# Kernel optimization log

Hardware: AMD Instinct MI355X
Metric: run time of the kernel (lower is better)

The kernel has to match this reference:

```python
import jax, jax.numpy as jnp
import numpy as np

N0 = 260000  # all sampled nodes (hop-2 sources)
N1 = 60000   # hop-1 targets / hop-2 sources
N2 = 10000   # final batch targets
E1 = 1500000
E2 = 250000
DIN, DH, DOUT = 128, 256, 128


def sage_conv(x_src, x_tgt, src, dst, n_tgt, Wl, b, Wr):
    # mean aggregation of source features over incoming edges per target,
    # then lin_l(agg) + lin_r(x_tgt)  (PyG SAGEConv default, lin_r has no bias)
    msg = x_src[src]                                             # [E, d]
    agg = jax.ops.segment_sum(msg, dst, num_segments=n_tgt)      # [n_tgt, d]
    cnt = jax.ops.segment_sum(jnp.ones((src.shape[0], 1), x_src.dtype), dst,
                              num_segments=n_tgt)                # [n_tgt, 1]
    agg = agg / jnp.maximum(cnt, 1.0)
    return agg @ Wl + b + x_tgt @ Wr


def setup_inputs() -> dict:
    key = jax.random.key(0)
    ks = jax.random.split(key, 10)
    s = 1.0 / np.sqrt(DIN)
    s2 = 1.0 / np.sqrt(DH)
    return {
        "x": jax.random.normal(ks[0], (N0, DIN), dtype=jnp.float32),
        "W1l": jax.random.normal(ks[1], (DIN, DH), dtype=jnp.float32) * s,
        "b1": jnp.zeros((DH,), dtype=jnp.float32),
        "W1r": jax.random.normal(ks[2], (DIN, DH), dtype=jnp.float32) * s,
        "W2l": jax.random.normal(ks[3], (DH, DOUT), dtype=jnp.float32) * s2,
        "b2": jnp.zeros((DOUT,), dtype=jnp.float32),
        "W2r": jax.random.normal(ks[4], (DH, DOUT), dtype=jnp.float32) * s2,
        "src1": jax.random.randint(ks[5], (E1,), 0, N0, dtype=jnp.int32),
        "dst1": jax.random.randint(ks[6], (E1,), 0, N1, dtype=jnp.int32),
        "src2": jax.random.randint(ks[7], (E2,), 0, N1, dtype=jnp.int32),
        "dst2": jax.random.randint(ks[8], (E2,), 0, N2, dtype=jnp.int32),
    }


def reference(x, W1l, b1, W1r, W2l, b2, W2r, src1, dst1, src2, dst2):
    h = sage_conv(x, x[:N1], src1, dst1, N1, W1l, b1, W1r)  # [N1, DH]
    h = jax.nn.relu(h)
    out = sage_conv(h, h[:N2], src2, dst2, N2, W2l, b2, W2r)  # [N2, DOUT]
    return out
```

## Files before the change

### kernel.cpp

```cpp
#include <hip/hip_runtime.h>
#include <hip/hip_bf16.h>

#define N0 260000
#define N1 60000
#define N2 10000
#define E1 1500000
#define E2 250000
#define DIN 128
#define DH 256
#define DOUT 128
#define CAP 80

typedef __attribute__((ext_vector_type(8))) short bf16x8;
typedef __attribute__((ext_vector_type(4))) float f32x4;

#define MFMA16(a, b, c) __builtin_amdgcn_mfma_f32_16x16x32_bf16(a, b, c, 0, 0, 0)

__device__ inline float blo(unsigned u) { return __uint_as_float(u << 16); }
__device__ inline float bhi(unsigned u) { return __uint_as_float(u & 0xFFFF0000u); }
__device__ inline unsigned short f2b(float f) {
    unsigned u = __float_as_uint(f);
    return (unsigned short)((u + 0x7FFFu + ((u >> 16) & 1u)) >> 16);
}

#define CONVX_BLOCKS 16250
#define CONVW_BLOCKS 512
__global__ __launch_bounds__(256) void prep2(const float* __restrict__ x, unsigned short* __restrict__ xb,
                                             const float* __restrict__ W1l, const float* __restrict__ W1r,
                                             const float* __restrict__ W2l, const float* __restrict__ W2r,
                                             unsigned short* __restrict__ W1lt, unsigned short* __restrict__ W1rt,
                                             unsigned short* __restrict__ W2lt, unsigned short* __restrict__ W2rt,
                                             int use_xb) {
    int b = blockIdx.x;
    int t = threadIdx.x;
    if (b < CONVX_BLOCKS) {
        if (!use_xb) return;
        size_t i = (size_t)b * 256 + t;
        const float4* xf = reinterpret_cast<const float4*>(x) + i * 2;
        float4 v0 = xf[0], v1 = xf[1];
        bf16x8 o;
        o[0] = (short)f2b(v0.x); o[1] = (short)f2b(v0.y); o[2] = (short)f2b(v0.z); o[3] = (short)f2b(v0.w);
        o[4] = (short)f2b(v1.x); o[5] = (short)f2b(v1.y); o[6] = (short)f2b(v1.z); o[7] = (short)f2b(v1.w);
        *reinterpret_cast<bf16x8*>(xb + i * 8) = o;
    } else {
        int tid = (b - CONVX_BLOCKS) * 256 + t;
        int seg = tid >> 15, idx = tid & 32767;
        if (seg == 0)      { int n = idx >> 7, k = idx & 127; W1lt[idx] = f2b(W1l[k * DH + n]); }
        else if (seg == 1) { int n = idx >> 7, k = idx & 127; W1rt[idx] = f2b(W1r[k * DH + n]); }
        else if (seg == 2) { int n = idx >> 8, k = idx & 255; W2lt[idx] = f2b(W2l[k * DOUT + n]); }
        else               { int n = idx >> 8, k = idx & 255; W2rt[idx] = f2b(W2r[k * DOUT + n]); }
    }
}

#define BB_C1 256
#define BB_C2 64
#define P1ROWS (N1 / 8)
#define P2ROWS (N2 / 8)
__global__ __launch_bounds__(256) void build_bucket(const int* __restrict__ src1, const int* __restrict__ dst1,
                                                    int* __restrict__ cnt1, int* __restrict__ csr1,
                                                    const int* __restrict__ src2, const int* __restrict__ dst2,
                                                    int* __restrict__ cnt2, int* __restrict__ csr2) {
    int b = blockIdx.x;
    int part = b & 7, q = b >> 3;
    int t = threadIdx.x;
    if (q < BB_C1) {
        int lo = part * P1ROWS, hi = lo + P1ROWS;
        const int4* d4 = reinterpret_cast<const int4*>(dst1);
        for (int i = q * 256 + t; i < E1 / 4; i += BB_C1 * 256) {
            int4 d = d4[i];
            int e0 = i * 4;
            if (d.x >= lo && d.x < hi) { int p = atomicAdd(&cnt1[d.x], 1); if (p < CAP) csr1[d.x * CAP + p] = src1[e0 + 0]; }
            if (d.y >= lo && d.y < hi) { int p = atomicAdd(&cnt1[d.y], 1); if (p < CAP) csr1[d.y * CAP + p] = src1[e0 + 1]; }
            if (d.z >= lo && d.z < hi) { int p = atomicAdd(&cnt1[d.z], 1); if (p < CAP) csr1[d.z * CAP + p] = src1[e0 + 2]; }
            if (d.w >= lo && d.w < hi) { int p = atomicAdd(&cnt1[d.w], 1); if (p < CAP) csr1[d.w * CAP + p] = src1[e0 + 3]; }
        }
    } else {
        q -= BB_C1;
        int lo = part * P2ROWS, hi = lo + P2ROWS;
        const int4* d4 = reinterpret_cast<const int4*>(dst2);
        for (int i = q * 256 + t; i < E2 / 4; i += BB_C2 * 256) {
            int4 d = d4[i];
            int e0 = i * 4;
            if (d.x >= lo && d.x < hi) { int p = atomicAdd(&cnt2[d.x], 1); if (p < CAP) csr2[d.x * CAP + p] = src2[e0 + 0]; }
            if (d.y >= lo && d.y < hi) { int p = atomicAdd(&cnt2[d.y], 1); if (p < CAP) csr2[d.y * CAP + p] = src2[e0 + 1]; }
            if (d.z >= lo && d.z < hi) { int p = atomicAdd(&cnt2[d.z], 1); if (p < CAP) csr2[d.z * CAP + p] = src2[e0 + 2]; }
            if (d.w >= lo && d.w < hi) { int p = atomicAdd(&cnt2[d.w], 1); if (p < CAP) csr2[d.w * CAP + p] = src2[e0 + 3]; }
        }
    }
}

template <int XB>
__global__ __launch_bounds__(256) void agg_gemm1_k(const float* __restrict__ xf,
                                                   const unsigned short* __restrict__ xb,
                                                   const int* __restrict__ cnt,
                                                   const int* __restrict__ csr,
                                                   const unsigned short* __restrict__ Wlt,
                                                   const unsigned short* __restrict__ Wrt,
                                                   const float* __restrict__ b1,
                                                   unsigned short* __restrict__ hb) {
    __shared__ __align__(16) unsigned short lds[4352];
    const int XT0 = 2176;
    int t = threadIdx.x;
    int row0 = blockIdx.x * 16;
    int r = t >> 4, li = t & 15;
    int rawc = cnt[row0 + r];
    int deg = rawc > CAP ? CAP : rawc;
    int beg = (row0 + r) * CAP, end = beg + deg;
    float acc[8];
#pragma unroll
    for (int j = 0; j < 8; ++j) acc[j] = 0.0f;
    if (XB) {
        const uint4* base = reinterpret_cast<const uint4*>(xb);
        int e = beg;
        for (; e + 4 <= end; e += 4) {
            int s0 = csr[e + 0];
            int s1 = csr[e + 1];
            int s2 = csr[e + 2];
            int s3 = csr[e + 3];
            uint4 v0 = base[(size_t)s0 * 16 + li];
            uint4 v1 = base[(size_t)s1 * 16 + li];
            uint4 v2 = base[(size_t)s2 * 16 + li];
            uint4 v3 = base[(size_t)s3 * 16 + li];
            acc[0] += blo(v0.x) + blo(v1.x) + blo(v2.x) + blo(v3.x);
            acc[1] += bhi(v0.x) + bhi(v1.x) + bhi(v2.x) + bhi(v3.x);
            acc[2] += blo(v0.y) + blo(v1.y) + blo(v2.y) + blo(v3.y);
            acc[3] += bhi(v0.y) + bhi(v1.y) + bhi(v2.y) + bhi(v3.y);
            acc[4] += blo(v0.z) + blo(v1.z) + blo(v2.z) + blo(v3.z);
            acc[5] += bhi(v0.z) + bhi(v1.z) + bhi(v2.z) + bhi(v3.z);
            acc[6] += blo(v0.w) + blo(v1.w) + blo(v2.w) + blo(v3.w);
            acc[7] += bhi(v0.w) + bhi(v1.w) + bhi(v2.w) + bhi(v3.w);
        }
        for (; e < end; ++e) {
            int s = csr[e];
            uint4 v = base[(size_t)s * 16 + li];
            acc[0] += blo(v.x); acc[1] += bhi(v.x);
            acc[2] += blo(v.y); acc[3] += bhi(v.y);
            acc[4] += blo(v.z); acc[5] += bhi(v.z);
            acc[6] += blo(v.w); acc[7] += bhi(v.w);
        }
    } else {
        const float4* base = reinterpret_cast<const float4*>(xf);
        for (int e = beg; e < end; ++e) {
            int s = csr[e];
            float4 v0 = base[(size_t)s * 32 + li * 2];
            float4 v1 = base[(size_t)s * 32 + li * 2 + 1];
            acc[0] += v0.x; acc[1] += v0.y; acc[2] += v0.z; acc[3] += v0.w;
            acc[4] += v1.x; acc[5] += v1.y; acc[6] += v1.z; acc[7] += v1.w;
        }
    }
    float inv = 1.0f / fmaxf((float)rawc, 1.0f);
    bf16x8 av;
#pragma unroll
    for (int j = 0; j < 8; ++j) av[j] = (short)f2b(acc[j] * inv);
    *reinterpret_cast<bf16x8*>(&lds[r * 136 + li * 8]) = av;
    if (XB) {
        *reinterpret_cast<uint4*>(&lds[XT0 + r * 136 + li * 8]) =
            reinterpret_cast<const uint4*>(xb)[(size_t)(row0 + r) * 16 + li];
    } else {
        const float4* base = reinterpret_cast<const float4*>(xf);
        float4 v0 = base[(size_t)(row0 + r) * 32 + li * 2];
        float4 v1 = base[(size_t)(row0 + r) * 32 + li * 2 + 1];
        bf16x8 xv;
        xv[0] = (short)f2b(v0.x); xv[1] = (short)f2b(v0.y); xv[2] = (short)f2b(v0.z); xv[3] = (short)f2b(v0.w);
        xv[4] = (short)f2b(v1.x); xv[5] = (short)f2b(v1.y); xv[6] = (short)f2b(v1.z); xv[7] = (short)f2b(v1.w);
        *reinterpret_cast<bf16x8*>(&lds[XT0 + r * 136 + li * 8]) = xv;
    }
    __syncthreads();

    int l = t & 63, w = t >> 6;
    f32x4 c[4];
#pragma unroll
    for (int nt = 0; nt < 4; ++nt) c[nt] = (f32x4){0.f, 0.f, 0.f, 0.f};
    int arow = (l & 15) * 136;
    int colbase = w * 64 + (l & 15);
    int kbase = (l >> 4) * 8;
#pragma unroll
    for (int kk = 0; kk < 4; ++kk) {
        int goff = arow + (kk * 4 + (l >> 4)) * 8;
        bf16x8 af = *reinterpret_cast<const bf16x8*>(&lds[goff]);
        bf16x8 tf = *reinterpret_cast<const bf16x8*>(&lds[XT0 + goff]);
        int k = kk * 32 + kbase;
#pragma unroll
        for (int nt = 0; nt < 4; ++nt) {
            int n = colbase + nt * 16;
            bf16x8 wl = *reinterpret_cast<const bf16x8*>(&Wlt[n * DIN + k]);
            bf16x8 wr = *reinterpret_cast<const bf16x8*>(&Wrt[n * DIN + k]);
            c[nt] = MFMA16(af, wl, c[nt]);
            c[nt] = MFMA16(tf, wr, c[nt]);
        }
    }
    __syncthreads();
#pragma unroll
    for (int nt = 0; nt < 4; ++nt) {
        int col = colbase + nt * 16;
        float bias = b1[col];
#pragma unroll
        for (int j = 0; j < 4; ++j) {
            int rr = (l >> 4) * 4 + j;
            lds[rr * 264 + col] = f2b(fmaxf(c[nt][j] + bias, 0.0f));
        }
    }
    __syncthreads();
#pragma unroll
    for (int i = 0; i < 2; ++i) {
        int gi = t + i * 256;
        int rr = gi >> 5, g = gi & 31;
        *reinterpret_cast<uint4*>(&hb[(size_t)(row0 + rr) * 256 + g * 8]) =
            *reinterpret_cast<const uint4*>(&lds[rr * 264 + g * 8]);
    }
}

__global__ __launch_bounds__(512) void agg_gemm2_k(const unsigned short* __restrict__ hb,
                                                   const int* __restrict__ cnt,
                                                   const int* __restrict__ csr,
                                                   const unsigned short* __restrict__ Wlt,
                                                   const unsigned short* __restrict__ Wrt,
                                                   const float* __restrict__ b2,
                                                   float* __restrict__ out) {
    __shared__ __align__(16) unsigned short lds[8448];
    const int HT0 = 4224;
    int t = threadIdx.x;
    int row0 = blockIdx.x * 16;
    int r = t >> 5, li = t & 31;
    int rawc = cnt[row0 + r];
    int deg = rawc > CAP ? CAP : rawc;
    int beg = (row0 + r) * CAP, end = beg + deg;
    float acc[8];
#pragma unroll
    for (int j = 0; j < 8; ++j) acc[j] = 0.0f;
    const uint4* base = reinterpret_cast<const uint4*>(hb);
    int e = beg;
    for (; e + 4 <= end; e += 4) {
        int s0 = csr[e + 0];
        int s1 = csr[e + 1];
        int s2 = csr[e + 2];
        int s3 = csr[e + 3];
        uint4 v0 = base[(size_t)s0 * 32 + li];
        uint4 v1 = base[(size_t)s1 * 32 + li];
        uint4 v2 = base[(size_t)s2 * 32 + li];
        uint4 v3 = base[(size_t)s3 * 32 + li];
        acc[0] += blo(v0.x) + blo(v1.x) + blo(v2.x) + blo(v3.x);
        acc[1] += bhi(v0.x) + bhi(v1.x) + bhi(v2.x) + bhi(v3.x);
        acc[2] += blo(v0.y) + blo(v1.y) + blo(v2.y) + blo(v3.y);
        acc[3] += bhi(v0.y) + bhi(v1.y) + bhi(v2.y) + bhi(v3.y);
        acc[4] += blo(v0.z) + blo(v1.z) + blo(v2.z) + blo(v3.z);
        acc[5] += bhi(v0.z) + bhi(v1.z) + bhi(v2.z) + bhi(v3.z);
        acc[6] += blo(v0.w) + blo(v1.w) + blo(v2.w) + blo(v3.w);
        acc[7] += bhi(v0.w) + bhi(v1.w) + bhi(v2.w) + bhi(v3.w);
    }
    for (; e < end; ++e) {
        int s = csr[e];
        uint4 v = base[(size_t)s * 32 + li];
        acc[0] += blo(v.x); acc[1] += bhi(v.x);
        acc[2] += blo(v.y); acc[3] += bhi(v.y);
        acc[4] += blo(v.z); acc[5] += bhi(v.z);
        acc[6] += blo(v.w); acc[7] += bhi(v.w);
    }
    float inv = 1.0f / fmaxf((float)rawc, 1.0f);
    bf16x8 av;
#pragma unroll
    for (int j = 0; j < 8; ++j) av[j] = (short)f2b(acc[j] * inv);
    *reinterpret_cast<bf16x8*>(&lds[r * 264 + li * 8]) = av;
    *reinterpret_cast<uint4*>(&lds[HT0 + r * 264 + li * 8]) =
        reinterpret_cast<const uint4*>(&hb[(size_t)(row0 + r) * 256])[li];
    __syncthreads();

    int l = t & 63, w = t >> 6;
    f32x4 c = (f32x4){0.f, 0.f, 0.f, 0.f};
    int arow = (l & 15) * 264;
    int col = w * 16 + (l & 15);
    int kbase = (l >> 4) * 8;
#pragma unroll
    for (int kk = 0; kk < 8; ++kk) {
        int goff = arow + (kk * 4 + (l >> 4)) * 8;
        bf16x8 af = *reinterpret_cast<const bf16x8*>(&lds[goff]);
        bf16x8 hf = *reinterpret_cast<const bf16x8*>(&lds[HT0 + goff]);
        int k = kk * 32 + kbase;
        bf16x8 wl = *reinterpret_cast<const bf16x8*>(&Wlt[col * DH + k]);
        bf16x8 wr = *reinterpret_cast<const bf16x8*>(&Wrt[col * DH + k]);
        c = MFMA16(af, wl, c);
        c = MFMA16(hf, wr, c);
    }
    __syncthreads();
    float* O = reinterpret_cast<float*>(lds);
    float bias = b2[col];
#pragma unroll
    for (int j = 0; j < 4; ++j) {
        int rr = (l >> 4) * 4 + j;
        O[rr * 132 + col] = c[j] + bias;
    }
    __syncthreads();
    {
        int rr = t >> 5, c4 = t & 31;
        reinterpret_cast<float4*>(&out[(size_t)(row0 + rr) * 128])[c4] =
            reinterpret_cast<const float4*>(O)[rr * 33 + c4];
    }
}

extern "C" void kernel_launch(void* const* d_in, const int* in_sizes, int n_in,
                              void* d_out, int out_size, void* d_ws, size_t ws_size,
                              hipStream_t stream) {
    const float* x   = (const float*)d_in[0];
    const float* W1l = (const float*)d_in[1];
    const float* b1  = (const float*)d_in[2];
    const float* W1r = (const float*)d_in[3];
    const float* W2l = (const float*)d_in[4];
    const float* b2  = (const float*)d_in[5];
    const float* W2r = (const float*)d_in[6];
    const int* src1  = (const int*)d_in[7];
    const int* dst1  = (const int*)d_in[8];
    const int* src2  = (const int*)d_in[9];
    const int* dst2  = (const int*)d_in[10];
    float* out = (float*)d_out;

    char* ws = (char*)d_ws;
    size_t off = 0;
    auto alloc = [&](size_t bytes) { void* p = ws + off; off += (bytes + 255) & ~(size_t)255; return p; };
    int* cnt1    = (int*)alloc((size_t)N1 * 4);
    int* cnt2    = (int*)alloc((size_t)N2 * 4);
    int* csr1    = (int*)alloc((size_t)N1 * CAP * 4);
    int* csr2    = (int*)alloc((size_t)N2 * CAP * 4);
    unsigned short* W1lt = (unsigned short*)alloc((size_t)DIN * DH * 2);
    unsigned short* W1rt = (unsigned short*)alloc((size_t)DIN * DH * 2);
    unsigned short* W2lt = (unsigned short*)alloc((size_t)DH * DOUT * 2);
    unsigned short* W2rt = (unsigned short*)alloc((size_t)DH * DOUT * 2);
    unsigned short* hb   = (unsigned short*)alloc((size_t)N1 * DH * 2);
    unsigned short* xb   = (unsigned short*)alloc((size_t)N0 * DIN * 2);
    int use_xb = (off <= ws_size) ? 1 : 0;

    hipMemsetAsync(cnt1, 0, (size_t)((char*)cnt2 - (char*)cnt1) + (size_t)N2 * 4, stream);

    prep2<<<CONVX_BLOCKS + CONVW_BLOCKS, 256, 0, stream>>>(
        x, xb, W1l, W1r, W2l, W2r, W1lt, W1rt, W2lt, W2rt, use_xb);

    build_bucket<<<8 * (BB_C1 + BB_C2), 256, 0, stream>>>(src1, dst1, cnt1, csr1,
                                                          src2, dst2, cnt2, csr2);

    if (use_xb)
        agg_gemm1_k<1><<<N1 / 16, 256, 0, stream>>>(x, xb, cnt1, csr1, W1lt, W1rt, b1, hb);
    else
        agg_gemm1_k<0><<<N1 / 16, 256, 0, stream>>>(x, nullptr, cnt1, csr1, W1lt, W1rt, b1, hb);

    agg_gemm2_k<<<N2 / 16, 512, 0, stream>>>(hb, cnt2, csr2, W2lt, W2rt, b2, out);
}
```

Baseline: 256.5 us.

## Fuse bucket build into prep kernel and widen gather unroll to eight edges

The CSR bucket-building work now runs as the leading blocks of the prep kernel, so the atomic scatter overlaps with the bf16 conversion of x and the weights, and one launch and its inter-kernel gap go away. Both aggregation kernels now read neighbour indices as int4 vectors and issue eight row gathers per iteration instead of four, with a four-edge tail step, to put more memory loads in flight. The vector index loads rely on each row's CSR slot being 16-byte aligned, which holds because CAP is 80. The wider unroll raises register use, which could lower occupancy.

Result: faster. 248.7 us (-3.1%).

```diff
diff --git a/kernel.cpp b/kernel.cpp
--- a/kernel.cpp
+++ b/kernel.cpp
@@ -23,19 +23,54 @@
     return (unsigned short)((u + 0x7FFFu + ((u >> 16) & 1u)) >> 16);
 }
 
+#define BB_C1 256
+#define BB_C2 64
+#define BB_BLOCKS (8 * (BB_C1 + BB_C2))
+#define P1ROWS (N1 / 8)
+#define P2ROWS (N2 / 8)
 #define CONVX_BLOCKS 16250
 #define CONVW_BLOCKS 512
-__global__ __launch_bounds__(256) void prep2(const float* __restrict__ x, unsigned short* __restrict__ xb,
+__global__ __launch_bounds__(256) void prep3(const float* __restrict__ x, unsigned short* __restrict__ xb,
                                              const float* __restrict__ W1l, const float* __restrict__ W1r,
                                              const float* __restrict__ W2l, const float* __restrict__ W2r,
                                              unsigned short* __restrict__ W1lt, unsigned short* __restrict__ W1rt,
                                              unsigned short* __restrict__ W2lt, unsigned short* __restrict__ W2rt,
+                                             const int* __restrict__ src1, const int* __restrict__ dst1,
+                                             int* __restrict__ cnt1, int* __restrict__ csr1,
+                                             const int* __restrict__ src2, const int* __restrict__ dst2,
+                                             int* __restrict__ cnt2, int* __restrict__ csr2,
                                              int use_xb) {
     int b = blockIdx.x;
     int t = threadIdx.x;
-    if (b < CONVX_BLOCKS) {
+    if (b < BB_BLOCKS) {
+        int part = b & 7, q = b >> 3;
+        if (q < BB_C1) {
+            int lo = part * P1ROWS, hi = lo + P1ROWS;
+            const int4* d4 = reinterpret_cast<const int4*>(dst1);
+            for (int i = q * 256 + t; i < E1 / 4; i += BB_C1 * 256) {
+                int4 d = d4[i];
+                int e0 = i * 4;
+                if (d.x >= lo && d.x < hi) { int p = atomicAdd(&cnt1[d.x], 1); if (p < CAP) csr1[d.x * CAP + p] = src1[e0 + 0]; }
+                if (d.y >= lo && d.y < hi) { int p = atomicAdd(&cnt1[d.y], 1); if (p < CAP) csr1[d.y * CAP + p] = src1[e0 + 1]; }
+                if (d.z >= lo && d.z < hi) { int p = atomicAdd(&cnt1[d.z], 1); if (p < CAP) csr1[d.z * CAP + p] = src1[e0 + 2]; }
+                if (d.w >= lo && d.w < hi) { int p = atomicAdd(&cnt1[d.w], 1); if (p < CAP) csr1[d.w * CAP + p] = src1[e0 + 3]; }
+            }
+        } else {
+            q -= BB_C1;
+            int lo = part * P2ROWS, hi = lo + P2ROWS;
+            const int4* d4 = reinterpret_cast<const int4*>(dst2);
+            for (int i = q * 256 + t; i < E2 / 4; i += BB_C2 * 256) {
+                int4 d = d4[i];
+                int e0 = i * 4;
+                if (d.x >= lo && d.x < hi) { int p = atomicAdd(&cnt2[d.x], 1); if (p < CAP) csr2[d.x * CAP + p] = src2[e0 + 0]; }
+                if (d.y >= lo && d.y < hi) { int p = atomicAdd(&cnt2[d.y], 1); if (p < CAP) csr2[d.y * CAP + p] = src2[e0 + 1]; }
+                if (d.z >= lo && d.z < hi) { int p = atomicAdd(&cnt2[d.z], 1); if (p < CAP) csr2[d.z * CAP + p] = src2[e0 + 2]; }
+                if (d.w >= lo && d.w < hi) { int p = atomicAdd(&cnt2[d.w], 1); if (p < CAP) csr2[d.w * CAP + p] = src2[e0 + 3]; }
+            }
+        }
+    } else if (b < BB_BLOCKS + CONVX_BLOCKS) {
         if (!use_xb) return;
-        size_t i = (size_t)b * 256 + t;
+        size_t i = (size_t)(b - BB_BLOCKS) * 256 + t;
         const float4* xf = reinterpret_cast<const float4*>(x) + i * 2;
         float4 v0 = xf[0], v1 = xf[1];
         bf16x8 o;
@@ -43,49 +78,12 @@
         o[4] = (short)f2b(v1.x); o[5] = (short)f2b(v1.y); o[6] = (short)f2b(v1.z); o[7] = (short)f2b(v1.w);
         *reinterpret_cast<bf16x8*>(xb + i * 8) = o;
     } else {
-        int tid = (b - CONVX_BLOCKS) * 256 + t;
+        int tid = (b - BB_BLOCKS - CONVX_BLOCKS) * 256 + t;
         int seg = tid >> 15, idx = tid & 32767;
         if (seg == 0)      { int n = idx >> 7, k = idx & 127; W1lt[idx] = f2b(W1l[k * DH + n]); }
         else if (seg == 1) { int n = idx >> 7, k = idx & 127; W1rt[idx] = f2b(W1r[k * DH + n]); }
         else if (seg == 2) { int n = idx >> 8, k = idx & 255; W2lt[idx] = f2b(W2l[k * DOUT + n]); }
         else               { int n = idx >> 8, k = idx & 255; W2rt[idx] = f2b(W2r[k * DOUT + n]); }
-    }
-}
-
-#define BB_C1 256
-#define BB_C2 64
-#define P1ROWS (N1 / 8)
-#define P2ROWS (N2 / 8)
-__global__ __launch_bounds__(256) void build_bucket(const int* __restrict__ src1, const int* __restrict__ dst1,
-                                                    int* __restrict__ cnt1, int* __restrict__ csr1,
-                                                    const int* __restrict__ src2, const int* __restrict__ dst2,
-                                                    int* __restrict__ cnt2, int* __restrict__ csr2) {
-    int b = blockIdx.x;
-    int part = b & 7, q = b >> 3;
-    int t = threadIdx.x;
-    if (q < BB_C1) {
-        int lo = part * P1ROWS, hi = lo + P1ROWS;
-        const int4* d4 = reinterpret_cast<const int4*>(dst1);
-        for (int i = q * 256 + t; i < E1 / 4; i += BB_C1 * 256) {
-            int4 d = d4[i];
-            int e0 = i * 4;
-            if (d.x >= lo && d.x < hi) { int p = atomicAdd(&cnt1[d.x], 1); if (p < CAP) csr1[d.x * CAP + p] = src1[e0 + 0]; }
-            if (d.y >= lo && d.y < hi) { int p = atomicAdd(&cnt1[d.y], 1); if (p < CAP) csr1[d.y * CAP + p] = src1[e0 + 1]; }
-            if (d.z >= lo && d.z < hi) { int p = atomicAdd(&cnt1[d.z], 1); if (p < CAP) csr1[d.z * CAP + p] = src1[e0 + 2]; }
-            if (d.w >= lo && d.w < hi) { int p = atomicAdd(&cnt1[d.w], 1); if (p < CAP) csr1[d.w * CAP + p] = src1[e0 + 3]; }
-        }
-    } else {
-        q -= BB_C1;
-        int lo = part * P2ROWS, hi = lo + P2ROWS;
-        const int4* d4 = reinterpret_cast<const int4*>(dst2);
-        for (int i = q * 256 + t; i < E2 / 4; i += BB_C2 * 256) {
-            int4 d = d4[i];
-            int e0 = i * 4;
-            if (d.x >= lo && d.x < hi) { int p = atomicAdd(&cnt2[d.x], 1); if (p < CAP) csr2[d.x * CAP + p] = src2[e0 + 0]; }
-            if (d.y >= lo && d.y < hi) { int p = atomicAdd(&cnt2[d.y], 1); if (p < CAP) csr2[d.y * CAP + p] = src2[e0 + 1]; }
-            if (d.z >= lo && d.z < hi) { int p = atomicAdd(&cnt2[d.z], 1); if (p < CAP) csr2[d.z * CAP + p] = src2[e0 + 2]; }
-            if (d.w >= lo && d.w < hi) { int p = atomicAdd(&cnt2[d.w], 1); if (p < CAP) csr2[d.w * CAP + p] = src2[e0 + 3]; }
-        }
     }
 }
 
@@ -112,15 +110,32 @@
     if (XB) {
         const uint4* base = reinterpret_cast<const uint4*>(xb);
         int e = beg;
-        for (; e + 4 <= end; e += 4) {
-            int s0 = csr[e + 0];
-            int s1 = csr[e + 1];
-            int s2 = csr[e + 2];
-            int s3 = csr[e + 3];
-            uint4 v0 = base[(size_t)s0 * 16 + li];
-            uint4 v1 = base[(size_t)s1 * 16 + li];
-            uint4 v2 = base[(size_t)s2 * 16 + li];
-            uint4 v3 = base[(size_t)s3 * 16 + li];
+        for (; e + 8 <= end; e += 8) {
+            int4 sa = *reinterpret_cast<const int4*>(csr + e);
+            int4 sb = *reinterpret_cast<const int4*>(csr + e + 4);
+            uint4 v0 = base[(size_t)sa.x * 16 + li];
+            uint4 v1 = base[(size_t)sa.y * 16 + li];
+            uint4 v2 = base[(size_t)sa.z * 16 + li];
+            uint4 v3 = base[(size_t)sa.w * 16 + li];
+            uint4 v4 = base[(size_t)sb.x * 16 + li];
+            uint4 v5 = base[(size_t)sb.y * 16 + li];
+            uint4 v6 = base[(size_t)sb.z * 16 + li];
+            uint4 v7 = base[(size_t)sb.w * 16 + li];
+            acc[0] += blo(v0.x) + blo(v1.x) + blo(v2.x) + blo(v3.x) + blo(v4.x) + blo(v5.x) + blo(v6.x) + blo(v7.x);
+            acc[1] += bhi(v0.x) + bhi(v1.x) + bhi(v2.x) + bhi(v3.x) + bhi(v4.x) + bhi(v5.x) + bhi(v6.x) + bhi(v7.x);
+            acc[2] += blo(v0.y) + blo(v1.y) + blo(v2.y) + blo(v3.y) + blo(v4.y) + blo(v5.y) + blo(v6.y) + blo(v7.y);
+            acc[3] += bhi(v0.y) + bhi(v1.y) + bhi(v2.y) + bhi(v3.y) + bhi(v4.y) + bhi(v5.y) + bhi(v6.y) + bhi(v7.y);
+            acc[4] += blo(v0.z) + blo(v1.z) + blo(v2.z) + blo(v3.z) + blo(v4.z) + blo(v5.z) + blo(v6.z) + blo(v7.z);
+            acc[5] += bhi(v0.z) + bhi(v1.z) + bhi(v2.z) + bhi(v3.z) + bhi(v4.z) + bhi(v5.z) + bhi(v6.z) + bhi(v7.z);
+            acc[6] += blo(v0.w) + blo(v1.w) + blo(v2.w) + blo(v3.w) + blo(v4.w) + blo(v5.w) + blo(v6.w) + blo(v7.w);
+            acc[7] += bhi(v0.w) + bhi(v1.w) + bhi(v2.w) + bhi(v3.w) + bhi(v4.w) + bhi(v5.w) + bhi(v6.w) + bhi(v7.w);
+        }
+        if (e + 4 <= end) {
+            int4 sa = *reinterpret_cast<const int4*>(csr + e);
+            uint4 v0 = base[(size_t)sa.x * 16 + li];
+            uint4 v1 = base[(size_t)sa.y * 16 + li];
+            uint4 v2 = base[(size_t)sa.z * 16 + li];
+            uint4 v3 = base[(size_t)sa.w * 16 + li];
             acc[0] += blo(v0.x) + blo(v1.x) + blo(v2.x) + blo(v3.x);
             acc[1] += bhi(v0.x) + bhi(v1.x) + bhi(v2.x) + bhi(v3.x);
             acc[2] += blo(v0.y) + blo(v1.y) + blo(v2.y) + blo(v3.y);
@@ -129,6 +144,7 @@
             acc[5] += bhi(v0.z) + bhi(v1.z) + bhi(v2.z) + bhi(v3.z);
             acc[6] += blo(v0.w) + blo(v1.w) + blo(v2.w) + blo(v3.w);
             acc[7] += bhi(v0.w) + bhi(v1.w) + bhi(v2.w) + bhi(v3.w);
+            e += 4;
         }
         for (; e < end; ++e) {
             int s = csr[e];
@@ -230,15 +246,32 @@
     for (int j = 0; j < 8; ++j) acc[j] = 0.0f;
     const uint4* base = reinterpret_cast<const uint4*>(hb);
     int e = beg;
-    for (; e + 4 <= end; e += 4) {
-        int s0 = csr[e + 0];
-        int s1 = csr[e + 1];
-        int s2 = csr[e + 2];
-        int s3 = csr[e + 3];
-        uint4 v0 = base[(size_t)s0 * 32 + li];
-        uint4 v1 = base[(size_t)s1 * 32 + li];
-        uint4 v2 = base[(size_t)s2 * 32 + li];
-        uint4 v3 = base[(size_t)s3 * 32 + li];
+    for (; e + 8 <= end; e += 8) {
+        int4 sa = *reinterpret_cast<const int4*>(csr + e);
+        int4 sb = *reinterpret_cast<const int4*>(csr + e + 4);
+        uint4 v0 = base[(size_t)sa.x * 32 + li];
+        uint4 v1 = base[(size_t)sa.y * 32 + li];
+        uint4 v2 = base[(size_t)sa.z * 32 + li];
+        uint4 v3 = base[(size_t)sa.w * 32 + li];
+        uint4 v4 = base[(size_t)sb.x * 32 + li];
+        uint4 v5 = base[(size_t)sb.y * 32 + li];
+        uint4 v6 = base[(size_t)sb.z * 32 + li];
+        uint4 v7 = base[(size_t)sb.w * 32 + li];
+        acc[0] += blo(v0.x) + blo(v1.x) + blo(v2.x) + blo(v3.x) + blo(v4.x) + blo(v5.x) + blo(v6.x) + blo(v7.x);
+        acc[1] += bhi(v0.x) + bhi(v1.x) + bhi(v2.x) + bhi(v3.x) + bhi(v4.x) + bhi(v5.x) + bhi(v6.x) + bhi(v7.x);
+        acc[2] += blo(v0.y) + blo(v1.y) + blo(v2.y) + blo(v3.y) + blo(v4.y) + blo(v5.y) + blo(v6.y) + blo(v7.y);
+        acc[3] += bhi(v0.y) + bhi(v1.y) + bhi(v2.y) + bhi(v3.y) + bhi(v4.y) + bhi(v5.y) + bhi(v6.y) + bhi(v7.y);
+        acc[4] += blo(v0.z) + blo(v1.z) + blo(v2.z) + blo(v3.z) + blo(v4.z) + blo(v5.z) + blo(v6.z) + blo(v7.z);
+        acc[5] += bhi(v0.z) + bhi(v1.z) + bhi(v2.z) + bhi(v3.z) + bhi(v4.z) + bhi(v5.z) + bhi(v6.z) + bhi(v7.z);
+        acc[6] += blo(v0.w) + blo(v1.w) + blo(v2.w) + blo(v3.w) + blo(v4.w) + blo(v5.w) + blo(v6.w) + blo(v7.w);
+        acc[7] += bhi(v0.w) + bhi(v1.w) + bhi(v2.w) + bhi(v3.w) + bhi(v4.w) + bhi(v5.w) + bhi(v6.w) + bhi(v7.w);
+    }
+    if (e + 4 <= end) {
+        int4 sa = *reinterpret_cast<const int4*>(csr + e);
+        uint4 v0 = base[(size_t)sa.x * 32 + li];
+        uint4 v1 = base[(size_t)sa.y * 32 + li];
+        uint4 v2 = base[(size_t)sa.z * 32 + li];
+        uint4 v3 = base[(size_t)sa.w * 32 + li];
         acc[0] += blo(v0.x) + blo(v1.x) + blo(v2.x) + blo(v3.x);
         acc[1] += bhi(v0.x) + bhi(v1.x) + bhi(v2.x) + bhi(v3.x);
         acc[2] += blo(v0.y) + blo(v1.y) + blo(v2.y) + blo(v3.y);
@@ -247,6 +280,7 @@
         acc[5] += bhi(v0.z) + bhi(v1.z) + bhi(v2.z) + bhi(v3.z);
         acc[6] += blo(v0.w) + blo(v1.w) + blo(v2.w) + blo(v3.w);
         acc[7] += bhi(v0.w) + bhi(v1.w) + bhi(v2.w) + bhi(v3.w);
+        e += 4;
     }
     for (; e < end; ++e) {
         int s = csr[e];
@@ -330,11 +364,9 @@
 
     hipMemsetAsync(cnt1, 0, (size_t)((char*)cnt2 - (char*)cnt1) + (size_t)N2 * 4, stream);
 
-    prep2<<<CONVX_BLOCKS + CONVW_BLOCKS, 256, 0, stream>>>(
-        x, xb, W1l, W1r, W2l, W2r, W1lt, W1rt, W2lt, W2rt, use_xb);
-
-    build_bucket<<<8 * (BB_C1 + BB_C2), 256, 0, stream>>>(src1, dst1, cnt1, csr1,
-                                                          src2, dst2, cnt2, csr2);
+    prep3<<<BB_BLOCKS + CONVX_BLOCKS + CONVW_BLOCKS, 256, 0, stream>>>(
+        x, xb, W1l, W1r, W2l, W2r, W1lt, W1rt, W2lt, W2rt,
+        src1, dst1, cnt1, csr1, src2, dst2, cnt2, csr2, use_xb);
 
     if (use_xb)
         agg_gemm1_k<1><<<N1 / 16, 256, 0, stream>>>(x, xb, cnt1, csr1, W1lt, W1rt, b1, hb);
```
